# Optimization experiments

Measured on AMD Instinct MI355X. Metric: run time of the kernel, lower is better.

The kernel has to match this reference:

```python
import jax, jax.numpy as jnp
import numpy as np

NUM_HEADS = 16
HEAD_DIM = 64  # d_out // num_heads = 1024 // 16


def setup_inputs() -> dict:
    key = jax.random.key(0)
    ks = jax.random.split(key, 9)
    B, S, D = 2, 2048, 1024
    scale = 0.02
    return {
        "x": jax.random.normal(ks[0], (B, S, D), jnp.float32),
        "Wq": jax.random.normal(ks[1], (D, D), jnp.float32) * scale,
        "bq": jax.random.normal(ks[2], (D,), jnp.float32) * scale,
        "Wk": jax.random.normal(ks[3], (D, D), jnp.float32) * scale,
        "bk": jax.random.normal(ks[4], (D,), jnp.float32) * scale,
        "Wv": jax.random.normal(ks[5], (D, D), jnp.float32) * scale,
        "bv": jax.random.normal(ks[6], (D,), jnp.float32) * scale,
        "Wo": jax.random.normal(ks[7], (D, D), jnp.float32) * scale,
        "bo": jax.random.normal(ks[8], (D,), jnp.float32) * scale,
    }


def reference(x, Wq, bq, Wk, bk, Wv, bv, Wo, bo):
    B, S, D = x.shape
    H, Dh = NUM_HEADS, HEAD_DIM
    # QKV projections (torch Linear: x @ W.T + b; here W stored as [d_in, d_out])
    q = (x @ Wq + bq).reshape(B, S, H, Dh).transpose(0, 2, 1, 3)  # [B,H,S,Dh]
    k = (x @ Wk + bk).reshape(B, S, H, Dh).transpose(0, 2, 1, 3)
    v = (x @ Wv + bv).reshape(B, S, H, Dh).transpose(0, 2, 1, 3)
    scores = jnp.einsum("bhqd,bhkd->bhqk", q, k)
    # causal mask applied before scaling (as in source; -inf unaffected by scale)
    causal = jnp.tril(jnp.ones((S, S), dtype=bool))
    scores = jnp.where(causal, scores, -jnp.inf) / jnp.sqrt(jnp.float32(Dh))
    attn = jax.nn.softmax(scores, axis=-1)  # dropout=0.0 (eval)
    ctx = jnp.einsum("bhqk,bhkd->bhqd", attn, v)  # [B,H,S,Dh]
    ctx = ctx.transpose(0, 2, 1, 3).reshape(B, S, D)
    return ctx @ Wo + bo
```

## Files before the change

### kernel.cpp

```cpp
#include <hip/hip_runtime.h>
#include <math.h>


#define H_  16
#define DH_ 64
#define D_  1024
#define S_  2048
#define B_  2

typedef __attribute__((ext_vector_type(8))) short short8;
typedef __attribute__((ext_vector_type(4))) float f32x4;

#define QSCALE 0.18033688011112042f
#define DEFER_THR 11.5416f

__device__ __forceinline__ unsigned short f2bf(float f) {
    union { float f; unsigned int u; } v; v.f = f;
    unsigned int r = (v.u + 0x7fffu + ((v.u >> 16) & 1u)) >> 16;
    return (unsigned short)r;
}

__device__ __forceinline__ float fast_exp2(float x) {
#if __has_builtin(__builtin_amdgcn_exp2f)
    return __builtin_amdgcn_exp2f(x);
#else
    return exp2f(x);
#endif
}

__device__ __forceinline__ void gload_lds16(const void* g, void* l) {
    __builtin_amdgcn_global_load_lds(
        (const __attribute__((address_space(1))) void*)g,
        (__attribute__((address_space(3))) void*)l, 16, 0, 0);
}

__global__ __launch_bounds__(256) void cvt_x_k(const float* __restrict__ x,
                                               unsigned short* __restrict__ xb)
{
    int i = (blockIdx.x * 256 + threadIdx.x) * 8;
    float4 a = *(const float4*)&x[i];
    float4 b = *(const float4*)&x[i + 4];
    uint4 o;
    o.x = f2bf(a.x) | ((unsigned)f2bf(a.y) << 16);
    o.y = f2bf(a.z) | ((unsigned)f2bf(a.w) << 16);
    o.z = f2bf(b.x) | ((unsigned)f2bf(b.y) << 16);
    o.w = f2bf(b.z) | ((unsigned)f2bf(b.w) << 16);
    *(uint4*)&xb[i] = o;
}

__global__ __launch_bounds__(256) void tr_w_k(
    const float* __restrict__ W0, const float* __restrict__ W1,
    const float* __restrict__ W2, const float* __restrict__ W3,
    unsigned short* __restrict__ wt)
{
    const float* W = W0;
    if (blockIdx.z == 1) W = W1; else if (blockIdx.z == 2) W = W2;
    else if (blockIdx.z == 3) W = W3;
    unsigned short* out = wt + (size_t)blockIdx.z * 1048576;

    __shared__ float t[64][65];
    const int k0 = blockIdx.x * 64, n0 = blockIdx.y * 64;
    const int r = threadIdx.x >> 4, c4 = (threadIdx.x & 15) * 4;

    #pragma unroll
    for (int p = 0; p < 4; ++p) {
        float4 v = *(const float4*)&W[(size_t)(k0 + r + 16 * p) * D_ + n0 + c4];
        t[r + 16 * p][c4 + 0] = v.x; t[r + 16 * p][c4 + 1] = v.y;
        t[r + 16 * p][c4 + 2] = v.z; t[r + 16 * p][c4 + 3] = v.w;
    }
    __syncthreads();
    #pragma unroll
    for (int p = 0; p < 4; ++p) {
        int nn = r + 16 * p;
        uint2 o;
        o.x = f2bf(t[c4 + 0][nn]) | ((unsigned)f2bf(t[c4 + 1][nn]) << 16);
        o.y = f2bf(t[c4 + 2][nn]) | ((unsigned)f2bf(t[c4 + 3][nn]) << 16);
        *(uint2*)&out[(size_t)(n0 + nn) * D_ + k0 + c4] = o;
    }
}

template<int QKV>
__global__ __launch_bounds__(256) void gemm_bf16(
    const unsigned short* __restrict__ Ab,
    const unsigned short* __restrict__ Wt,
    const float* __restrict__ b0, const float* __restrict__ b1,
    const float* __restrict__ b2,
    void* __restrict__ o0, void* __restrict__ o1, void* __restrict__ o2)
{
    const unsigned short* W = Wt;
    const float* bias = b0;
    int z = 0;
    if (QKV) {
        z = blockIdx.z;
        W = Wt + (size_t)z * 1048576;
        if (z == 1) bias = b1; else if (z == 2) bias = b2;
    }
    const int n0 = blockIdx.x * 128, j0 = blockIdx.y * 128;
    const int tid = threadIdx.x;
    const int lane = tid & 63;
    const int wq = tid >> 6, wm = wq >> 1, wn = wq & 1;
    const int lr = lane & 15, lk = lane >> 4;

    __shared__ __align__(16) char smem[32768];

    f32x4 acc[4][4] = {};

    for (int k0 = 0; k0 < D_; k0 += 64) {
        __syncthreads();
        #pragma unroll
        for (int c = 0; c < 4; ++c) {
            int u = c * 256 + tid;
            int r = u >> 3, sp = u & 7, sl = sp ^ (r & 7);
            gload_lds16(&Ab[(size_t)(n0 + r) * D_ + k0 + sl * 8], &smem[u * 16]);
        }
        #pragma unroll
        for (int c = 0; c < 4; ++c) {
            int u = c * 256 + tid;
            int r = u >> 3, sp = u & 7, sl = sp ^ (r & 7);
            gload_lds16(&W[(size_t)(j0 + r) * D_ + k0 + sl * 8],
                        &smem[16384 + u * 16]);
        }
        __syncthreads();
        #pragma unroll
        for (int kc = 0; kc < 2; ++kc) {
            short8 a[4], b[4];
            #pragma unroll
            for (int m = 0; m < 4; ++m) {
                int row = wm * 64 + m * 16 + lr;
                int sp = (kc * 4 + lk) ^ (row & 7);
                a[m] = *(const short8*)&smem[row * 128 + sp * 16];
            }
            #pragma unroll
            for (int n = 0; n < 4; ++n) {
                int row = wn * 64 + n * 16 + lr;
                int sp = (kc * 4 + lk) ^ (row & 7);
                b[n] = *(const short8*)&smem[16384 + row * 128 + sp * 16];
            }
            #pragma unroll
            for (int m = 0; m < 4; ++m)
                #pragma unroll
                for (int n = 0; n < 4; ++n)
                    acc[m][n] = __builtin_amdgcn_mfma_f32_16x16x32_bf16(
                        a[m], b[n], acc[m][n], 0, 0, 0);
        }
    }

    float bn[4];
    #pragma unroll
    for (int n = 0; n < 4; ++n) bn[n] = bias[j0 + wn * 64 + n * 16 + lr];

    if (QKV) {
        __syncthreads();
        char* ep = smem + wq * 8192;
        const int head = (j0 + wn * 64) >> 6;
        const int row0 = n0 + wm * 64;
        const float sc = (z == 0) ? QSCALE : 1.0f;

        if (z < 2) {
            #pragma unroll
            for (int m = 0; m < 4; ++m)
                #pragma unroll
                for (int n = 0; n < 4; ++n) {
                    int col = n * 16 + lr;
                    #pragma unroll
                    for (int r = 0; r < 4; ++r) {
                        int row = m * 16 + lk * 4 + r;
                        int phys = (col >> 3) ^ (row & 7);
                        *(unsigned short*)&ep[row * 128 + phys * 16 + (col & 7) * 2]
                            = f2bf((acc[m][n][r] + bn[n]) * sc);
                    }
                }
            unsigned short* out = (unsigned short*)(z == 0 ? o0 : o1);
            #pragma unroll
            for (int p8 = 0; p8 < 8; ++p8) {
                int row = p8 * 8 + (lane >> 3);
                int phys = (lane & 7) ^ (row & 7);
                uint4 pk = *(const uint4*)&ep[row * 128 + phys * 16];
                int nrow = row0 + row;
                int bb = nrow >> 11, s = nrow & (S_ - 1);
                *(uint4*)&out[(((size_t)(bb * H_ + head)) * S_ + s) * 64
                              + (lane & 7) * 8] = pk;
            }
        } else {
            #pragma unroll
            for (int m = 0; m < 4; ++m)
                #pragma unroll
                for (int n = 0; n < 4; ++n) {
                    int row = n * 16 + lr;
                    #pragma unroll
                    for (int r = 0; r < 4; ++r) {
                        int col = m * 16 + lk * 4 + r;
                        int phys = (col >> 3) ^ (row & 7);
                        *(unsigned short*)&ep[row * 128 + phys * 16 + (col & 7) * 2]
                            = f2bf(acc[m][n][r] + bn[n]);
                    }
                }
            unsigned short* out = (unsigned short*)o2;
            int bb = row0 >> 11, s0 = row0 & (S_ - 1);
            #pragma unroll
            for (int p8 = 0; p8 < 8; ++p8) {
                int dh = p8 * 8 + (lane >> 3);
                int phys = (lane & 7) ^ (dh & 7);
                uint4 pk = *(const uint4*)&ep[dh * 128 + phys * 16];
                *(uint4*)&out[(((size_t)(bb * H_ + head)) * 64 + dh) * S_
                              + s0 + (lane & 7) * 8] = pk;
            }
        }
    } else {
        float* out = (float*)o0;
        #pragma unroll
        for (int m = 0; m < 4; ++m)
            #pragma unroll
            for (int n = 0; n < 4; ++n) {
                int col = j0 + wn * 64 + n * 16 + lr;
                int row0 = n0 + wm * 64 + m * 16 + lk * 4;
                #pragma unroll
                for (int r = 0; r < 4; ++r)
                    out[(size_t)(row0 + r) * D_ + col] = acc[m][n][r] + bn[n];
            }
    }
}

__global__ __launch_bounds__(256) void attn_mfma(
    const unsigned short* __restrict__ q, const unsigned short* __restrict__ k,
    const unsigned short* __restrict__ vt, unsigned short* __restrict__ ctx)
{
    const int bh = blockIdx.x;
    const int tid = threadIdx.x;
    const int lane = tid & 63, wq = tid >> 6;
    const int lx = lane & 15, hi = lane >> 4;

    __shared__ __align__(16) char smem[24576];
    char* Pw = &smem[16384 + wq * 2048];

    const int b = bh >> 4, h = bh & (H_ - 1);

    for (int half = 0; half < 2; ++half) {
        const int qt = half ? blockIdx.y : 31 - blockIdx.y;

        short8 qf[2];
        {
            const unsigned short* qrow =
                q + ((size_t)bh * S_ + qt * 64 + wq * 16 + lx) * 64;
            qf[0] = *(const short8*)&qrow[hi * 8];
            qf[1] = *(const short8*)&qrow[32 + hi * 8];
        }

        f32x4 o[4] = {};
        float m = -INFINITY, l = 0.f;
        const int qg = qt * 64 + wq * 16 + lx;

        for (int kt = 0; kt <= qt; ++kt) {
            __syncthreads();
            #pragma unroll
            for (int c = 0; c < 2; ++c) {
                int u = c * 256 + tid;
                int r = u >> 3, sp = u & 7, sl = sp ^ (r & 7);
                gload_lds16(&k[((size_t)bh * S_ + kt * 64 + r) * 64 + sl * 8],
                            &smem[u * 16]);
            }
            #pragma unroll
            for (int c = 0; c < 2; ++c) {
                int u = c * 256 + tid;
                int r = u >> 3, sp = u & 7, sl = sp ^ (r & 7);
                gload_lds16(&vt[((size_t)bh * 64 + r) * S_ + kt * 64 + sl * 8],
                            &smem[8192 + u * 16]);
            }
            __syncthreads();

            f32x4 s[4] = {};
            #pragma unroll
            for (int rt = 0; rt < 4; ++rt) {
                #pragma unroll
                for (int ks = 0; ks < 2; ++ks) {
                    int row = rt * 16 + lx;
                    int sp = (ks * 4 + hi) ^ (row & 7);
                    short8 kf = *(const short8*)&smem[row * 128 + sp * 16];
                    s[rt] = __builtin_amdgcn_mfma_f32_16x16x32_bf16(
                        kf, qf[ks], s[rt], 0, 0, 0);
                }
            }

            if (kt == qt) {
                #pragma unroll
                for (int rt = 0; rt < 4; ++rt)
                    #pragma unroll
                    for (int r = 0; r < 4; ++r) {
                        int kvg = kt * 64 + rt * 16 + hi * 4 + r;
                        if (kvg > qg) s[rt][r] = -INFINITY;
                    }
            }

            float tmax = s[0][0];
            #pragma unroll
            for (int rt = 0; rt < 4; ++rt)
                tmax = fmaxf(tmax, fmaxf(fmaxf(s[rt][0], s[rt][1]),
                                         fmaxf(s[rt][2], s[rt][3])));
            tmax = fmaxf(tmax, __shfl_xor(tmax, 16));
            tmax = fmaxf(tmax, __shfl_xor(tmax, 32));

            if (__any(tmax > m + DEFER_THR)) {
                float mn = fmaxf(m, tmax);
                float corr = fast_exp2(m - mn);
                m = mn;
                float ps = 0.f;
                #pragma unroll
                for (int rt = 0; rt < 4; ++rt)
                    #pragma unroll
                    for (int r = 0; r < 4; ++r) {
                        s[rt][r] = fast_exp2(s[rt][r] - mn);
                        ps += s[rt][r];
                    }
                ps += __shfl_xor(ps, 16);
                ps += __shfl_xor(ps, 32);
                l = l * corr + ps;
                #pragma unroll
                for (int r = 0; r < 4; ++r) {
                    float cr = __shfl(corr, hi * 4 + r);
                    #pragma unroll
                    for (int ct = 0; ct < 4; ++ct) o[ct][r] *= cr;
                }
            } else {
                float ps = 0.f;
                #pragma unroll
                for (int rt = 0; rt < 4; ++rt)
                    #pragma unroll
                    for (int r = 0; r < 4; ++r) {
                        s[rt][r] = fast_exp2(s[rt][r] - m);
                        ps += s[rt][r];
                    }
                ps += __shfl_xor(ps, 16);
                ps += __shfl_xor(ps, 32);
                l += ps;
            }

            #pragma unroll
            for (int rt = 0; rt < 4; ++rt) {
                uint2 pk;
                pk.x = f2bf(s[rt][0]) | ((unsigned)f2bf(s[rt][1]) << 16);
                pk.y = f2bf(s[rt][2]) | ((unsigned)f2bf(s[rt][3]) << 16);
                int sl = 2 * rt + (hi >> 1);
                *(uint2*)&Pw[lx * 128 + ((sl ^ (lx & 7)) * 16) + (hi & 1) * 8] = pk;
            }
            short8 pf[2];
            #pragma unroll
            for (int ks = 0; ks < 2; ++ks) {
                int sl = ks * 4 + hi;
                pf[ks] = *(const short8*)&Pw[lx * 128 + ((sl ^ (lx & 7)) * 16)];
            }

            #pragma unroll
            for (int ct = 0; ct < 4; ++ct) {
                #pragma unroll
                for (int ks = 0; ks < 2; ++ks) {
                    int row = ct * 16 + lx;
                    int sp = (ks * 4 + hi) ^ (row & 7);
                    short8 vf = *(const short8*)&smem[8192 + row * 128 + sp * 16];
                    o[ct] = __builtin_amdgcn_mfma_f32_16x16x32_bf16(
                        pf[ks], vf, o[ct], 0, 0, 0);
                }
            }
        }

        #pragma unroll
        for (int r = 0; r < 4; ++r) {
            float inv = 1.0f / __shfl(l, hi * 4 + r);
            int srow = qt * 64 + wq * 16 + hi * 4 + r;
            #pragma unroll
            for (int ct = 0; ct < 4; ++ct)
                ctx[((size_t)(b * S_ + srow)) * D_ + h * 64 + ct * 16 + lx] =
                    f2bf(o[ct][r] * inv);
        }
        __syncthreads();
    }
}

extern "C" void kernel_launch(void* const* d_in, const int* in_sizes, int n_in,
                              void* d_out, int out_size, void* d_ws, size_t ws_size,
                              hipStream_t stream)
{
    const float* x  = (const float*)d_in[0];
    const float* Wq = (const float*)d_in[1];
    const float* bq = (const float*)d_in[2];
    const float* Wk = (const float*)d_in[3];
    const float* bk = (const float*)d_in[4];
    const float* Wv = (const float*)d_in[5];
    const float* bv = (const float*)d_in[6];
    const float* Wo = (const float*)d_in[7];
    const float* bo = (const float*)d_in[8];
    float* out = (float*)d_out;

    const size_t per = (size_t)B_ * H_ * S_ * DH_;
    unsigned short* qb  = (unsigned short*)d_ws;
    unsigned short* kb  = qb + per;
    unsigned short* vtb = kb + per;
    unsigned short* xb  = vtb + per;
    unsigned short* wt  = xb + per;
    unsigned short* cb  = xb;

    cvt_x_k<<<2048, 256, 0, stream>>>(x, xb);
    tr_w_k<<<dim3(16, 16, 4), 256, 0, stream>>>(Wq, Wk, Wv, Wo, wt);

    gemm_bf16<1><<<dim3(32, 8, 3), 256, 0, stream>>>(
        xb, wt, bq, bk, bv, qb, kb, vtb);

    attn_mfma<<<dim3(32, 16), 256, 0, stream>>>(qb, kb, vtb, cb);

    gemm_bf16<0><<<dim3(32, 8, 1), 256, 0, stream>>>(
        cb, wt + 3u * 1048576u, bo, nullptr, nullptr, out, nullptr, nullptr);
}
```

Baseline: 199.6 us.

## Double-buffer K/V tiles in attention and launch one query tile per block

The attention kernel now prefetches the next K and V^T tile into a second LDS buffer while computing on the current one, with a single waitcnt+barrier per iteration replacing two syncthreads. The paired causal-balancing loop (two query tiles per block) is removed in favour of a 32x32 grid with one tile per block, which gives more, but unevenly sized, blocks. P is packed to bf16 with the hardware v_cvt_pk_bf16_f32 instruction instead of software rounding. LDS use grows from 24 KB to 40 KB per block, which may reduce occupancy.

```diff
diff --git a/kernel.cpp b/kernel.cpp
--- a/kernel.cpp
+++ b/kernel.cpp
@@ -18,6 +18,12 @@
     union { float f; unsigned int u; } v; v.f = f;
     unsigned int r = (v.u + 0x7fffu + ((v.u >> 16) & 1u)) >> 16;
     return (unsigned short)r;
+}
+
+__device__ __forceinline__ unsigned cvt_pk_bf16(float lo, float hi) {
+    unsigned r;
+    asm("v_cvt_pk_bf16_f32 %0, %1, %2" : "=v"(r) : "v"(lo), "v"(hi));
+    return r;
 }
 
 __device__ __forceinline__ float fast_exp2(float x) {
@@ -33,6 +39,8 @@
         (const __attribute__((address_space(1))) void*)g,
         (__attribute__((address_space(3))) void*)l, 16, 0, 0);
 }
+
+#define SYNC_VM0() asm volatile("s_waitcnt vmcnt(0)\n\ts_barrier" ::: "memory")
 
 __global__ __launch_bounds__(256) void cvt_x_k(const float* __restrict__ x,
                                                unsigned short* __restrict__ xb)
@@ -226,152 +234,172 @@
     const unsigned short* __restrict__ vt, unsigned short* __restrict__ ctx)
 {
     const int bh = blockIdx.x;
+    const int qt = 31 - blockIdx.y;
     const int tid = threadIdx.x;
     const int lane = tid & 63, wq = tid >> 6;
     const int lx = lane & 15, hi = lane >> 4;
 
-    __shared__ __align__(16) char smem[24576];
-    char* Pw = &smem[16384 + wq * 2048];
+    __shared__ __align__(16) char smem[40960];
+    char* Pw = &smem[32768 + wq * 2048];
 
     const int b = bh >> 4, h = bh & (H_ - 1);
 
-    for (int half = 0; half < 2; ++half) {
-        const int qt = half ? blockIdx.y : 31 - blockIdx.y;
-
-        short8 qf[2];
-        {
-            const unsigned short* qrow =
-                q + ((size_t)bh * S_ + qt * 64 + wq * 16 + lx) * 64;
-            qf[0] = *(const short8*)&qrow[hi * 8];
-            qf[1] = *(const short8*)&qrow[32 + hi * 8];
-        }
-
-        f32x4 o[4] = {};
-        float m = -INFINITY, l = 0.f;
-        const int qg = qt * 64 + wq * 16 + lx;
-
-        for (int kt = 0; kt <= qt; ++kt) {
-            __syncthreads();
+    short8 qf[2];
+    {
+        const unsigned short* qrow =
+            q + ((size_t)bh * S_ + qt * 64 + wq * 16 + lx) * 64;
+        qf[0] = *(const short8*)&qrow[hi * 8];
+        qf[1] = *(const short8*)&qrow[32 + hi * 8];
+    }
+
+    f32x4 o[4] = {};
+    float m = -INFINITY, l = 0.f;
+    const int qg = qt * 64 + wq * 16 + lx;
+
+    {
+        #pragma unroll
+        for (int c = 0; c < 2; ++c) {
+            int u = c * 256 + tid;
+            int r = u >> 3, sp = u & 7, sl = sp ^ (r & 7);
+            gload_lds16(&k[((size_t)bh * S_ + r) * 64 + sl * 8], &smem[u * 16]);
+        }
+        #pragma unroll
+        for (int c = 0; c < 2; ++c) {
+            int u = c * 256 + tid;
+            int r = u >> 3, sp = u & 7, sl = sp ^ (r & 7);
+            gload_lds16(&vt[((size_t)bh * 64 + r) * S_ + sl * 8],
+                        &smem[8192 + u * 16]);
+        }
+    }
+    SYNC_VM0();
+
+    int cur = 0;
+    for (int kt = 0; kt <= qt; ++kt) {
+        char* bufc = smem + cur * 16384;
+
+        if (kt < qt) {
+            char* bufn = smem + (cur ^ 1) * 16384;
             #pragma unroll
             for (int c = 0; c < 2; ++c) {
                 int u = c * 256 + tid;
                 int r = u >> 3, sp = u & 7, sl = sp ^ (r & 7);
-                gload_lds16(&k[((size_t)bh * S_ + kt * 64 + r) * 64 + sl * 8],
-                            &smem[u * 16]);
+                gload_lds16(&k[((size_t)bh * S_ + (kt + 1) * 64 + r) * 64 + sl * 8],
+                            &bufn[u * 16]);
             }
             #pragma unroll
             for (int c = 0; c < 2; ++c) {
                 int u = c * 256 + tid;
                 int r = u >> 3, sp = u & 7, sl = sp ^ (r & 7);
-                gload_lds16(&vt[((size_t)bh * 64 + r) * S_ + kt * 64 + sl * 8],
-                            &smem[8192 + u * 16]);
-            }
-            __syncthreads();
-
-            f32x4 s[4] = {};
-            #pragma unroll
-            for (int rt = 0; rt < 4; ++rt) {
-                #pragma unroll
-                for (int ks = 0; ks < 2; ++ks) {
-                    int row = rt * 16 + lx;
-                    int sp = (ks * 4 + hi) ^ (row & 7);
-                    short8 kf = *(const short8*)&smem[row * 128 + sp * 16];
-                    s[rt] = __builtin_amdgcn_mfma_f32_16x16x32_bf16(
-                        kf, qf[ks], s[rt], 0, 0, 0);
+                gload_lds16(&vt[((size_t)bh * 64 + r) * S_ + (kt + 1) * 64 + sl * 8],
+                            &bufn[8192 + u * 16]);
+            }
+        }
+
+        f32x4 s[4] = {};
+        #pragma unroll
+        for (int rt = 0; rt < 4; ++rt) {
+            #pragma unroll
+            for (int ks = 0; ks < 2; ++ks) {
+                int row = rt * 16 + lx;
+                int sp = (ks * 4 + hi) ^ (row & 7);
+                short8 kf = *(const short8*)&bufc[row * 128 + sp * 16];
+                s[rt] = __builtin_amdgcn_mfma_f32_16x16x32_bf16(
+                    kf, qf[ks], s[rt], 0, 0, 0);
+            }
+        }
+
+        if (kt == qt) {
+            #pragma unroll
+            for (int rt = 0; rt < 4; ++rt)
+                #pragma unroll
+                for (int r = 0; r < 4; ++r) {
+                    int kvg = kt * 64 + rt * 16 + hi * 4 + r;
+                    if (kvg > qg) s[rt][r] = -INFINITY;
                 }
-            }
-
-            if (kt == qt) {
-                #pragma unroll
-                for (int rt = 0; rt < 4; ++rt)
-                    #pragma unroll
-                    for (int r = 0; r < 4; ++r) {
-                        int kvg = kt * 64 + rt * 16 + hi * 4 + r;
-                        if (kvg > qg) s[rt][r] = -INFINITY;
-                    }
-            }
-
-            float tmax = s[0][0];
+        }
+
+        float tmax = s[0][0];
+        #pragma unroll
+        for (int rt = 0; rt < 4; ++rt)
+            tmax = fmaxf(tmax, fmaxf(fmaxf(s[rt][0], s[rt][1]),
+                                     fmaxf(s[rt][2], s[rt][3])));
+        tmax = fmaxf(tmax, __shfl_xor(tmax, 16));
+        tmax = fmaxf(tmax, __shfl_xor(tmax, 32));
+
+        if (__any(tmax > m + DEFER_THR)) {
+            float mn = fmaxf(m, tmax);
+            float corr = fast_exp2(m - mn);
+            m = mn;
+            float ps = 0.f;
             #pragma unroll
             for (int rt = 0; rt < 4; ++rt)
-                tmax = fmaxf(tmax, fmaxf(fmaxf(s[rt][0], s[rt][1]),
-                                         fmaxf(s[rt][2], s[rt][3])));
-            tmax = fmaxf(tmax, __shfl_xor(tmax, 16));
-            tmax = fmaxf(tmax, __shfl_xor(tmax, 32));
-
-            if (__any(tmax > m + DEFER_THR)) {
-                float mn = fmaxf(m, tmax);
-                float corr = fast_exp2(m - mn);
-                m = mn;
-                float ps = 0.f;
-                #pragma unroll
-                for (int rt = 0; rt < 4; ++rt)
-                    #pragma unroll
-                    for (int r = 0; r < 4; ++r) {
-                        s[rt][r] = fast_exp2(s[rt][r] - mn);
-                        ps += s[rt][r];
-                    }
-                ps += __shfl_xor(ps, 16);
-                ps += __shfl_xor(ps, 32);
-                l = l * corr + ps;
                 #pragma unroll
                 for (int r = 0; r < 4; ++r) {
-                    float cr = __shfl(corr, hi * 4 + r);
-                    #pragma unroll
-                    for (int ct = 0; ct < 4; ++ct) o[ct][r] *= cr;
+                    s[rt][r] = fast_exp2(s[rt][r] - mn);
+                    ps += s[rt][r];
                 }
-            } else {
-                float ps = 0.f;
-                #pragma unroll
-                for (int rt = 0; rt < 4; ++rt)
-                    #pragma unroll
-                    for (int r = 0; r < 4; ++r) {
-                        s[rt][r] = fast_exp2(s[rt][r] - m);
-                        ps += s[rt][r];
-                    }
-                ps += __shfl_xor(ps, 16);
-                ps += __shfl_xor(ps, 32);
-                l += ps;
-            }
-
-            #pragma unroll
-            for (int rt = 0; rt < 4; ++rt) {
-                uint2 pk;
-                pk.x = f2bf(s[rt][0]) | ((unsigned)f2bf(s[rt][1]) << 16);
-                pk.y = f2bf(s[rt][2]) | ((unsigned)f2bf(s[rt][3]) << 16);
-                int sl = 2 * rt + (hi >> 1);
-                *(uint2*)&Pw[lx * 128 + ((sl ^ (lx & 7)) * 16) + (hi & 1) * 8] = pk;
-            }
-            short8 pf[2];
+            ps += __shfl_xor(ps, 16);
+            ps += __shfl_xor(ps, 32);
+            l = l * corr + ps;
+            #pragma unroll
+            for (int r = 0; r < 4; ++r) {
+                float cr = __shfl(corr, hi * 4 + r);
+                #pragma unroll
+                for (int ct = 0; ct < 4; ++ct) o[ct][r] *= cr;
+            }
+        } else {
+            float ps = 0.f;
+            #pragma unroll
+            for (int rt = 0; rt < 4; ++rt)
+                #pragma unroll
+                for (int r = 0; r < 4; ++r) {
+                    s[rt][r] = fast_exp2(s[rt][r] - m);
+                    ps += s[rt][r];
+                }
+            ps += __shfl_xor(ps, 16);
+            ps += __shfl_xor(ps, 32);
+            l += ps;
+        }
+
+        #pragma unroll
+        for (int rt = 0; rt < 4; ++rt) {
+            uint2 pk;
+            pk.x = cvt_pk_bf16(s[rt][0], s[rt][1]);
+            pk.y = cvt_pk_bf16(s[rt][2], s[rt][3]);
+            int sl = 2 * rt + (hi >> 1);
+            *(uint2*)&Pw[lx * 128 + ((sl ^ (lx & 7)) * 16) + (hi & 1) * 8] = pk;
+        }
+        short8 pf[2];
+        #pragma unroll
+        for (int ks = 0; ks < 2; ++ks) {
+            int sl = ks * 4 + hi;
+            pf[ks] = *(const short8*)&Pw[lx * 128 + ((sl ^ (lx & 7)) * 16)];
+        }
+
+        #pragma unroll
+        for (int ct = 0; ct < 4; ++ct) {
             #pragma unroll
             for (int ks = 0; ks < 2; ++ks) {
-                int sl = ks * 4 + hi;
-                pf[ks] = *(const short8*)&Pw[lx * 128 + ((sl ^ (lx & 7)) * 16)];
-            }
-
-            #pragma unroll
-            for (int ct = 0; ct < 4; ++ct) {
-                #pragma unroll
-                for (int ks = 0; ks < 2; ++ks) {
-                    int row = ct * 16 + lx;
-                    int sp = (ks * 4 + hi) ^ (row & 7);
-                    short8 vf = *(const short8*)&smem[8192 + row * 128 + sp * 16];
-                    o[ct] = __builtin_amdgcn_mfma_f32_16x16x32_bf16(
-                        pf[ks], vf, o[ct], 0, 0, 0);
-                }
-            }
-        }
-
-        #pragma unroll
-        for (int r = 0; r < 4; ++r) {
-            float inv = 1.0f / __shfl(l, hi * 4 + r);
-            int srow = qt * 64 + wq * 16 + hi * 4 + r;
-            #pragma unroll
-            for (int ct = 0; ct < 4; ++ct)
-                ctx[((size_t)(b * S_ + srow)) * D_ + h * 64 + ct * 16 + lx] =
-                    f2bf(o[ct][r] * inv);
-        }
-        __syncthreads();
+                int row = ct * 16 + lx;
+                int sp = (ks * 4 + hi) ^ (row & 7);
+                short8 vf = *(const short8*)&bufc[8192 + row * 128 + sp * 16];
+                o[ct] = __builtin_amdgcn_mfma_f32_16x16x32_bf16(
+                    pf[ks], vf, o[ct], 0, 0, 0);
+            }
+        }
+
+        SYNC_VM0();
+        cur ^= 1;
+    }
+
+    #pragma unroll
+    for (int r = 0; r < 4; ++r) {
+        float inv = 1.0f / __shfl(l, hi * 4 + r);
+        int srow = qt * 64 + wq * 16 + hi * 4 + r;
+        #pragma unroll
+        for (int ct = 0; ct < 4; ++ct)
+            ctx[((size_t)(b * S_ + srow)) * D_ + h * 64 + ct * 16 + lx] =
+                f2bf(o[ct][r] * inv);
     }
 }
 
@@ -404,7 +432,7 @@
     gemm_bf16<1><<<dim3(32, 8, 3), 256, 0, stream>>>(
         xb, wt, bq, bk, bv, qb, kb, vtb);
 
-    attn_mfma<<<dim3(32, 16), 256, 0, stream>>>(qb, kb, vtb, cb);
+    attn_mfma<<<dim3(32, 32), 256, 0, stream>>>(qb, kb, vtb, cb);
 
     gemm_bf16<0><<<dim3(32, 8, 1), 256, 0, stream>>>(
         cb, wt + 3u * 1048576u, bo, nullptr, nullptr, out, nullptr, nullptr);
```

After: 197.5 us. About the same (-1.1%).
